# Optimization experiments

Hardware: AMD Instinct MI355X
Metric: run time of the kernel (lower is better)

Reference implementation:

```python
import jax, jax.numpy as jnp
import numpy as np

N, IN, OUT, T = 500000, 128, 64, 8

def setup_inputs() -> dict:
    key = jax.random.key(0)
    k1, k2, k3, k4 = jax.random.split(key, 4)
    x = jax.random.normal(k1, (N, IN), dtype=jnp.float32)
    node_type = jax.random.randint(k2, (N,), 0, T, dtype=jnp.int32)
    # per-type Linear weights, stored as [T, IN, OUT] so x @ W[t] matches torch Linear
    W = jax.random.normal(k3, (T, IN, OUT), dtype=jnp.float32) * (1.0 / np.sqrt(IN))
    b = jax.random.normal(k4, (T, OUT), dtype=jnp.float32) * 0.01
    return {"x": x, "node_type": node_type, "W": W, "b": b}

def reference(x, node_type, W, b):
    # emb_x[mask_t] = x[mask_t] @ W[t] + b[t], for each node type t.
    # Vectorized: loop over the small fixed number of types, masked accumulate.
    T_ = W.shape[0]
    out = jnp.zeros((x.shape[0], W.shape[2]), dtype=x.dtype)
    for t in range(T_):
        y_t = x @ W[t] + b[t]                      # [N, OUT]
        mask = (node_type == t)[:, None]           # [N, 1]
        out = jnp.where(mask, y_t, out)
    return out
```

## Files before the change

kernel.cpp:

```cpp
#include <hip/hip_runtime.h>
#include <hip/hip_bf16.h>

#define NT   8
#define INF  128
#define OUTF 64

typedef __attribute__((ext_vector_type(8))) short short8;
typedef __attribute__((ext_vector_type(4))) float f32x4;

__device__ __forceinline__ short f2bf(float f) {
  __hip_bfloat16 h = __float2bfloat16(f);
  return __builtin_bit_cast(short, h);
}


__global__ void hl_hist(const int* __restrict__ nt, int* __restrict__ ws, int N) {
  __shared__ int bins[NT];
  if (threadIdx.x < NT) bins[threadIdx.x] = 0;
  __syncthreads();
  const int N4 = N >> 2;
  const int4* p = (const int4*)nt;
  for (int i = blockIdx.x * blockDim.x + threadIdx.x; i < N4; i += gridDim.x * blockDim.x) {
    int4 v = p[i];
    atomicAdd(&bins[v.x], 1); atomicAdd(&bins[v.y], 1);
    atomicAdd(&bins[v.z], 1); atomicAdd(&bins[v.w], 1);
  }
  if (blockIdx.x == 0 && threadIdx.x < (N & 3))
    atomicAdd(&bins[nt[N4 * 4 + threadIdx.x]], 1);
  __syncthreads();
  if (threadIdx.x < NT) atomicAdd(&ws[threadIdx.x], bins[threadIdx.x]);
}

__global__ void hl_prefix(int* __restrict__ ws) {
  if (threadIdx.x == 0) {
    int s = 0;
    for (int t = 0; t < NT; ++t) { ws[8 + t] = s; ws[24 + t] = s; s += ws[t]; }
    ws[16] = s;
  }
}

#define SCHUNK 2048
__global__ void hl_scatter(const int* __restrict__ nt, int* __restrict__ ws, int N) {
  __shared__ int bins[NT], base[NT];
  int* cursor = ws + 24;
  int* perm   = ws + 32;
  if (threadIdx.x < NT) bins[threadIdx.x] = 0;
  __syncthreads();
  const int n0 = blockIdx.x * SCHUNK + threadIdx.x * 8;
  int ty[8], rk[8];
  #pragma unroll
  for (int i = 0; i < 8; ++i) {
    int n = n0 + i;
    if (n < N) { int t = nt[n]; ty[i] = t; rk[i] = atomicAdd(&bins[t], 1); }
    else ty[i] = -1;
  }
  __syncthreads();
  if (threadIdx.x < NT) base[threadIdx.x] = atomicAdd(&cursor[threadIdx.x], bins[threadIdx.x]);
  __syncthreads();
  #pragma unroll
  for (int i = 0; i < 8; ++i)
    if (ty[i] >= 0) perm[base[ty[i]] + rk[i]] = n0 + i;
}

__global__ __launch_bounds__(256) void hl_gemm(
    const float* __restrict__ x, const float* __restrict__ W,
    const float* __restrict__ b, const int* __restrict__ ws,
    float* __restrict__ out) {
  const int* start = ws + 8;
  const int* perm  = ws + 32;
  const int t  = blockIdx.y;
  const int s0 = start[t], s1 = start[t + 1];
  const int count = s1 - s0;
  if (count <= 0) return;
  const int ntiles = (count + 15) >> 4;
  if ((int)(blockIdx.x * 4) >= ntiles) return;

  const int wave = threadIdx.x >> 6;
  const int lane = threadIdx.x & 63;
  const int q = lane >> 4, c = lane & 15;

  short8 wf[4][4];
  const float* Wt = W + t * INF * OUTF;
  #pragma unroll
  for (int s = 0; s < 4; ++s)
    #pragma unroll
    for (int nb = 0; nb < 4; ++nb) {
      short8 v;
      #pragma unroll
      for (int j = 0; j < 8; ++j)
        v[j] = f2bf(Wt[(s * 32 + q * 8 + j) * OUTF + nb * 16 + c]);
      wf[s][nb] = v;
    }
  float bias[4];
  #pragma unroll
  for (int nb = 0; nb < 4; ++nb) bias[nb] = b[t * OUTF + nb * 16 + c];

  for (int tile = blockIdx.x * 4 + wave; tile < ntiles; tile += gridDim.x * 4) {
    const int rowbase = s0 + tile * 16;
    int ra = rowbase + c; if (ra > s1 - 1) ra = s1 - 1;
    const int na = perm[ra];
    const float* xr = x + (long)na * INF;
    f32x4 xv[4][2];
    #pragma unroll
    for (int s = 0; s < 4; ++s) {
      xv[s][0] = *(const f32x4*)(xr + s * 32 + q * 8);
      xv[s][1] = *(const f32x4*)(xr + s * 32 + q * 8 + 4);
    }
    short8 af[4];
    #pragma unroll
    for (int s = 0; s < 4; ++s)
      #pragma unroll
      for (int j = 0; j < 4; ++j) {
        af[s][j]     = f2bf(xv[s][0][j]);
        af[s][j + 4] = f2bf(xv[s][1][j]);
      }
    f32x4 acc[4] = {{0,0,0,0},{0,0,0,0},{0,0,0,0},{0,0,0,0}};
    #pragma unroll
    for (int s = 0; s < 4; ++s)
      #pragma unroll
      for (int nb = 0; nb < 4; ++nb)
        acc[nb] = __builtin_amdgcn_mfma_f32_16x16x32_bf16(af[s], wf[s][nb], acc[nb], 0, 0, 0);
    const int rb = rowbase + q * 4;
    #pragma unroll
    for (int r = 0; r < 4; ++r) {
      const int rowi = rb + r;
      if (rowi < s1) {
        const int node = perm[rowi];
        float* orow = out + (long)node * OUTF + c;
        #pragma unroll
        for (int nb = 0; nb < 4; ++nb)
          orow[nb * 16] = acc[nb][r] + bias[nb];
      }
    }
  }
}

extern "C" void kernel_launch(void* const* d_in, const int* in_sizes, int n_in,
                              void* d_out, int out_size, void* d_ws, size_t ws_size,
                              hipStream_t stream) {
  const float* x  = (const float*)d_in[0];
  const int*   nt = (const int*)d_in[1];
  const float* W  = (const float*)d_in[2];
  const float* b  = (const float*)d_in[3];
  float* out = (float*)d_out;
  const int N = in_sizes[1];
  int* ws = (int*)d_ws;

  hipMemsetAsync(ws, 0, 32 * sizeof(int), stream);
  hl_hist<<<256, 256, 0, stream>>>(nt, ws, N);
  hl_prefix<<<1, 64, 0, stream>>>(ws);
  hl_scatter<<<(N + SCHUNK - 1) / SCHUNK, 256, 0, stream>>>(nt, ws, N);
  dim3 grid(128, NT);
  hl_gemm<<<grid, 256, 0, stream>>>(x, W, b, ws, out);
}
```

Before: 441.9 us.

## Replace type-sorted gather GEMM with dense masked all-type MFMA pass

Drops the histogram/prefix/scatter permutation pipeline and instead processes rows in natural order, running MFMAs for all 8 types with the A fragment zeroed for rows of other types. Weights are pre-converted to bf16 fragment layout by a small kernel and streamed from cache inside the loop. This removes gathered x reads and scattered output writes plus several kernel launches, at the cost of 8x redundant matrix math and per-tile weight reloads.

```diff
diff --git a/kernel.cpp b/kernel.cpp
--- a/kernel.cpp
+++ b/kernel.cpp
@@ -13,123 +13,106 @@
   return __builtin_bit_cast(short, h);
 }
 
-
-__global__ void hl_hist(const int* __restrict__ nt, int* __restrict__ ws, int N) {
-  __shared__ int bins[NT];
-  if (threadIdx.x < NT) bins[threadIdx.x] = 0;
-  __syncthreads();
-  const int N4 = N >> 2;
-  const int4* p = (const int4*)nt;
-  for (int i = blockIdx.x * blockDim.x + threadIdx.x; i < N4; i += gridDim.x * blockDim.x) {
-    int4 v = p[i];
-    atomicAdd(&bins[v.x], 1); atomicAdd(&bins[v.y], 1);
-    atomicAdd(&bins[v.z], 1); atomicAdd(&bins[v.w], 1);
-  }
-  if (blockIdx.x == 0 && threadIdx.x < (N & 3))
-    atomicAdd(&bins[nt[N4 * 4 + threadIdx.x]], 1);
-  __syncthreads();
-  if (threadIdx.x < NT) atomicAdd(&ws[threadIdx.x], bins[threadIdx.x]);
+__global__ void hl_wconv(const float* __restrict__ W, short* __restrict__ wbf) {
+  const int tid   = blockIdx.x * blockDim.x + threadIdx.x;
+  const int combo = tid >> 6;
+  const int lane  = tid & 63;
+  const int t = combo >> 4, s = (combo >> 2) & 3, nb = combo & 3;
+  const int q = lane >> 4, c = lane & 15;
+  const float* Wt = W + t * INF * OUTF;
+  short8 v;
+  #pragma unroll
+  for (int j = 0; j < 8; ++j)
+    v[j] = f2bf(Wt[(s * 32 + q * 8 + j) * OUTF + nb * 16 + c]);
+  *(short8*)(wbf + (size_t)tid * 8) = v;
 }
 
-__global__ void hl_prefix(int* __restrict__ ws) {
-  if (threadIdx.x == 0) {
-    int s = 0;
-    for (int t = 0; t < NT; ++t) { ws[8 + t] = s; ws[24 + t] = s; s += ws[t]; }
-    ws[16] = s;
-  }
-}
-
-#define SCHUNK 2048
-__global__ void hl_scatter(const int* __restrict__ nt, int* __restrict__ ws, int N) {
-  __shared__ int bins[NT], base[NT];
-  int* cursor = ws + 24;
-  int* perm   = ws + 32;
-  if (threadIdx.x < NT) bins[threadIdx.x] = 0;
-  __syncthreads();
-  const int n0 = blockIdx.x * SCHUNK + threadIdx.x * 8;
-  int ty[8], rk[8];
-  #pragma unroll
-  for (int i = 0; i < 8; ++i) {
-    int n = n0 + i;
-    if (n < N) { int t = nt[n]; ty[i] = t; rk[i] = atomicAdd(&bins[t], 1); }
-    else ty[i] = -1;
-  }
-  __syncthreads();
-  if (threadIdx.x < NT) base[threadIdx.x] = atomicAdd(&cursor[threadIdx.x], bins[threadIdx.x]);
-  __syncthreads();
-  #pragma unroll
-  for (int i = 0; i < 8; ++i)
-    if (ty[i] >= 0) perm[base[ty[i]] + rk[i]] = n0 + i;
-}
-
-__global__ __launch_bounds__(256) void hl_gemm(
-    const float* __restrict__ x, const float* __restrict__ W,
-    const float* __restrict__ b, const int* __restrict__ ws,
-    float* __restrict__ out) {
-  const int* start = ws + 8;
-  const int* perm  = ws + 32;
-  const int t  = blockIdx.y;
-  const int s0 = start[t], s1 = start[t + 1];
-  const int count = s1 - s0;
-  if (count <= 0) return;
-  const int ntiles = (count + 15) >> 4;
-  if ((int)(blockIdx.x * 4) >= ntiles) return;
-
+__global__ __launch_bounds__(256) void hl_main(
+    const float* __restrict__ x, const int* __restrict__ nty,
+    const short* __restrict__ wbf, const float* __restrict__ b,
+    float* __restrict__ out, int N) {
+  const int ntiles = (N + 15) >> 4;
   const int wave = threadIdx.x >> 6;
   const int lane = threadIdx.x & 63;
   const int q = lane >> 4, c = lane & 15;
+  const int nwaves = gridDim.x * 4;
+  const short* wp = wbf + (size_t)lane * 8;
 
-  short8 wf[4][4];
-  const float* Wt = W + t * INF * OUTF;
-  #pragma unroll
-  for (int s = 0; s < 4; ++s)
-    #pragma unroll
-    for (int nb = 0; nb < 4; ++nb) {
-      short8 v;
-      #pragma unroll
-      for (int j = 0; j < 8; ++j)
-        v[j] = f2bf(Wt[(s * 32 + q * 8 + j) * OUTF + nb * 16 + c]);
-      wf[s][nb] = v;
-    }
-  float bias[4];
-  #pragma unroll
-  for (int nb = 0; nb < 4; ++nb) bias[nb] = b[t * OUTF + nb * 16 + c];
+  for (int tile = blockIdx.x * 4 + wave; tile < ntiles; tile += nwaves) {
+    const int base = tile * 16;
+    int rowa = base + c; if (rowa > N - 1) rowa = N - 1;
+    const int ty = nty[rowa];
+    const float* xr = x + (size_t)rowa * INF;
 
-  for (int tile = blockIdx.x * 4 + wave; tile < ntiles; tile += gridDim.x * 4) {
-    const int rowbase = s0 + tile * 16;
-    int ra = rowbase + c; if (ra > s1 - 1) ra = s1 - 1;
-    const int na = perm[ra];
-    const float* xr = x + (long)na * INF;
-    f32x4 xv[4][2];
+    short8 A[4];
     #pragma unroll
     for (int s = 0; s < 4; ++s) {
-      xv[s][0] = *(const f32x4*)(xr + s * 32 + q * 8);
-      xv[s][1] = *(const f32x4*)(xr + s * 32 + q * 8 + 4);
+      f32x4 v0 = *(const f32x4*)(xr + s * 32 + q * 8);
+      f32x4 v1 = *(const f32x4*)(xr + s * 32 + q * 8 + 4);
+      short8 a;
+      #pragma unroll
+      for (int j = 0; j < 4; ++j) { a[j] = f2bf(v0[j]); a[j + 4] = f2bf(v1[j]); }
+      A[s] = a;
     }
-    short8 af[4];
+
+    f32x4 acc[4] = {{0,0,0,0},{0,0,0,0},{0,0,0,0},{0,0,0,0}};
+    const short8 z8 = {0,0,0,0,0,0,0,0};
+
+    short8 BA[4], BB[4];
     #pragma unroll
-    for (int s = 0; s < 4; ++s)
+    for (int nb = 0; nb < 4; ++nb) BA[nb] = *(const short8*)(wp + (size_t)nb * 512);
+
+    #pragma unroll 1
+    for (int t = 0; t < NT; ++t) {
+      const int f0 = t * 16;
+      const int fn = (f0 + 16 < 128) ? f0 + 16 : 124;
       #pragma unroll
-      for (int j = 0; j < 4; ++j) {
-        af[s][j]     = f2bf(xv[s][0][j]);
-        af[s][j + 4] = f2bf(xv[s][1][j]);
-      }
-    f32x4 acc[4] = {{0,0,0,0},{0,0,0,0},{0,0,0,0},{0,0,0,0}};
-    #pragma unroll
-    for (int s = 0; s < 4; ++s)
+      for (int nb = 0; nb < 4; ++nb) BB[nb] = *(const short8*)(wp + (size_t)(f0 + 4 + nb) * 512);
+      { short8 am = (ty == t) ? A[0] : z8;
+        #pragma unroll
+        for (int nb = 0; nb < 4; ++nb)
+          acc[nb] = __builtin_amdgcn_mfma_f32_16x16x32_bf16(am, BA[nb], acc[nb], 0, 0, 0); }
       #pragma unroll
-      for (int nb = 0; nb < 4; ++nb)
-        acc[nb] = __builtin_amdgcn_mfma_f32_16x16x32_bf16(af[s], wf[s][nb], acc[nb], 0, 0, 0);
-    const int rb = rowbase + q * 4;
+      for (int nb = 0; nb < 4; ++nb) BA[nb] = *(const short8*)(wp + (size_t)(f0 + 8 + nb) * 512);
+      { short8 am = (ty == t) ? A[1] : z8;
+        #pragma unroll
+        for (int nb = 0; nb < 4; ++nb)
+          acc[nb] = __builtin_amdgcn_mfma_f32_16x16x32_bf16(am, BB[nb], acc[nb], 0, 0, 0); }
+      #pragma unroll
+      for (int nb = 0; nb < 4; ++nb) BB[nb] = *(const short8*)(wp + (size_t)(f0 + 12 + nb) * 512);
+      { short8 am = (ty == t) ? A[2] : z8;
+        #pragma unroll
+        for (int nb = 0; nb < 4; ++nb)
+          acc[nb] = __builtin_amdgcn_mfma_f32_16x16x32_bf16(am, BA[nb], acc[nb], 0, 0, 0); }
+      #pragma unroll
+      for (int nb = 0; nb < 4; ++nb) BA[nb] = *(const short8*)(wp + (size_t)(fn + nb) * 512);
+      { short8 am = (ty == t) ? A[3] : z8;
+        #pragma unroll
+        for (int nb = 0; nb < 4; ++nb)
+          acc[nb] = __builtin_amdgcn_mfma_f32_16x16x32_bf16(am, BB[nb], acc[nb], 0, 0, 0); }
+    }
+
+    const int rbase = base + q * 4;
+    int4 tyv;
+    if (rbase + 3 < N) {
+      tyv = *(const int4*)(nty + rbase);
+    } else {
+      int t0 = rbase + 0 < N ? nty[rbase + 0] : 0;
+      int t1 = rbase + 1 < N ? nty[rbase + 1] : 0;
+      int t2 = rbase + 2 < N ? nty[rbase + 2] : 0;
+      int t3 = rbase + 3 < N ? nty[rbase + 3] : 0;
+      tyv.x = t0; tyv.y = t1; tyv.z = t2; tyv.w = t3;
+    }
+    const int trs[4] = {tyv.x, tyv.y, tyv.z, tyv.w};
     #pragma unroll
     for (int r = 0; r < 4; ++r) {
-      const int rowi = rb + r;
-      if (rowi < s1) {
-        const int node = perm[rowi];
-        float* orow = out + (long)node * OUTF + c;
+      const int row = rbase + r;
+      if (row < N) {
+        const float* br = b + trs[r] * OUTF + c;
+        float* orow = out + (size_t)row * OUTF + c;
         #pragma unroll
         for (int nb = 0; nb < 4; ++nb)
-          orow[nb * 16] = acc[nb][r] + bias[nb];
+          orow[nb * 16] = acc[nb][r] + br[nb * 16];
       }
     }
   }
@@ -144,12 +127,8 @@
   const float* b  = (const float*)d_in[3];
   float* out = (float*)d_out;
   const int N = in_sizes[1];
-  int* ws = (int*)d_ws;
+  short* wbf = (short*)d_ws;
 
-  hipMemsetAsync(ws, 0, 32 * sizeof(int), stream);
-  hl_hist<<<256, 256, 0, stream>>>(nt, ws, N);
-  hl_prefix<<<1, 64, 0, stream>>>(ws);
-  hl_scatter<<<(N + SCHUNK - 1) / SCHUNK, 256, 0, stream>>>(nt, ws, N);
-  dim3 grid(128, NT);
-  hl_gemm<<<grid, 256, 0, stream>>>(x, W, b, ws, out);
+  hl_wconv<<<32, 256, 0, stream>>>(W, wbf);
+  hl_main<<<2048, 256, 0, stream>>>(x, nt, wbf, b, out, N);
 }
```

Result: slower. 479.6 us (+8.5%).
